# Kernel optimization log

Hardware: AMD Instinct MI355X
Metric: run time of the kernel (lower is better)

## Reference

```python
import jax, jax.numpy as jnp
import numpy as np

N, E, G = 25600, 409600, 128   # nodes, edges, graphs
IN, H, C = 200, 4, 64          # raw feat dim, heads, hidden_channels
IN2 = 2 * IN                   # after NaN-mask concat
BN_EPS = 1e-5

def _glorot(key, shape):
    lim = float(np.sqrt(6.0 / (shape[0] + shape[-1])))
    return jax.random.uniform(key, shape, jnp.float32, -lim, lim)

def setup_inputs():
    key = jax.random.key(0)
    k = iter(jax.random.split(key, 40))
    inp = {
        "x": jax.random.normal(next(k), (N, IN), jnp.float32),
        "edge_index": jax.random.randint(next(k), (2, E), 0, N, jnp.int32),
        "edge_attr": jax.random.normal(next(k), (E, 1), jnp.float32),
        "batch": jnp.repeat(jnp.arange(G, dtype=jnp.int32), N // G),
    }
    dims = [(IN2, H, C), (H * C, H, C), (H * C, 1, C)]
    for i, (din, h, c) in enumerate(dims):
        inp[f"W{i}"] = _glorot(next(k), (din, h * c))
        inp[f"as{i}"] = _glorot(next(k), (h, c))
        inp[f"ad{i}"] = _glorot(next(k), (h, c))
        inp[f"We{i}"] = _glorot(next(k), (1, h * c))
        inp[f"ae{i}"] = _glorot(next(k), (h, c))
        inp[f"b{i}"] = jnp.zeros((h * c,), jnp.float32)
    inp["bn_g"] = jnp.ones((H * C,), jnp.float32)
    inp["bn_b"] = jnp.zeros((H * C,), jnp.float32)
    inp["bn_m"] = jnp.zeros((H * C,), jnp.float32)
    inp["bn_v"] = jnp.ones((H * C,), jnp.float32)
    inp["cw1"] = _glorot(next(k), (C, C))
    inp["cb1"] = jnp.zeros((C,), jnp.float32)
    inp["cw2"] = _glorot(next(k), (C, 2))
    inp["cb2"] = jnp.zeros((2,), jnp.float32)
    return inp

def _gat(x, src, dst, ea, W, att_s, att_d, We, att_e, b, heads, ch):
    """PyG GATConv (edge_dim=1, add_self_loops=True, fill_value='mean', concat=True)."""
    n = x.shape[0]
    # self-loop edge_attr = mean of incoming edge_attr per destination node
    cnt = jax.ops.segment_sum(jnp.ones((ea.shape[0], 1), ea.dtype), dst, n)
    loop_ea = jax.ops.segment_sum(ea, dst, n) / jnp.maximum(cnt, 1.0)
    idx = jnp.arange(n, dtype=src.dtype)
    src = jnp.concatenate([src, idx])
    dst = jnp.concatenate([dst, idx])
    ea = jnp.concatenate([ea, loop_ea], axis=0)
    h = (x @ W).reshape(n, heads, ch)                      # [N,H,C]
    a_s = jnp.einsum('nhc,hc->nh', h, att_s)
    a_d = jnp.einsum('nhc,hc->nh', h, att_d)
    a_e = jnp.einsum('ehc,hc->eh', (ea @ We).reshape(-1, heads, ch), att_e)
    alpha = jax.nn.leaky_relu(a_s[src] + a_d[dst] + a_e, 0.2)   # [E',H]
    # segment softmax over destination neighborhoods
    m = jax.ops.segment_max(alpha, dst, n)
    ex = jnp.exp(alpha - m[dst])
    z = jax.ops.segment_sum(ex, dst, n)
    alpha = ex / (z[dst] + 1e-16)
    out = jax.ops.segment_sum(h[src] * alpha[:, :, None], dst, n)  # [N,H,C]
    return out.reshape(n, heads * ch) + b

def reference(x, edge_index, edge_attr, batch,
              W0, as0, ad0, We0, ae0, b0,
              W1, as1, ad1, We1, ae1, b1,
              W2, as2, ad2, We2, ae2, b2,
              bn_g, bn_b, bn_m, bn_v, cw1, cb1, cw2, cb2):
    nan_mask = jnp.isnan(x).astype(x.dtype)
    x = jnp.concatenate([jnp.nan_to_num(x), nan_mask], axis=-1)   # [N, 2*IN]
    edge_attr = jnp.nan_to_num(edge_attr)
    src, dst = edge_index[0], edge_index[1]
    for (W, a_s, a_d, We, a_e, b) in [(W0, as0, ad0, We0, ae0, b0),
                                      (W1, as1, ad1, We1, ae1, b1)]:
        x = _gat(x, src, dst, edge_attr, W, a_s, a_d, We, a_e, b, H, C)
        x = (x - bn_m) / jnp.sqrt(bn_v + BN_EPS) * bn_g + bn_b    # eval-mode BN
        x = jax.nn.relu(x)                                        # dropout = identity (eval)
    x = _gat(x, src, dst, edge_attr, W2, as2, ad2, We2, ae2, b2, 1, C)
    # global mean pool over graphs
    cnt = jax.ops.segment_sum(jnp.ones((x.shape[0], 1), x.dtype), batch, G)
    g = jax.ops.segment_sum(x, batch, G) / jnp.maximum(cnt, 1.0)  # [G, C]
    hdn = jax.nn.gelu(g @ cw1 + cb1, approximate=False)
    return hdn @ cw2 + cb2                                        # [G, 2]
```

## Files before the change

### kernel.cpp

```cpp
#include <hip/hip_runtime.h>
#include <hip/hip_bf16.h>

static const int kN  = 25600;
static const int kE  = 409600;
static const int kG  = 128;
static const int kNPG = 200;
static const int kIN = 200;
static const int kIN2 = 400;
static const int kHB = 64;
static const int kEPB = kE / kHB;
#define BN_EPS_ 1e-5f

typedef __attribute__((ext_vector_type(8))) short short8;
typedef __attribute__((ext_vector_type(4))) ushort us4;
typedef __attribute__((ext_vector_type(4))) float f32x4;

__device__ __forceinline__ float bu(ushort u) {
  union { float f; unsigned u32; } x; x.u32 = ((unsigned)u) << 16; return x.f;
}
__device__ __forceinline__ ushort f2u(float v) {
  __hip_bfloat16 t = __float2bfloat16(v);
  return *(ushort*)&t;
}
__device__ __forceinline__ float wredSum(float v) {
#pragma unroll
  for (int off = 1; off < 64; off <<= 1) v += __shfl_xor(v, off, 64);
  return v;
}
__device__ __forceinline__ float lrelu(float a) { return (a > 0.f) ? a : 0.2f * a; }

__global__ void k_pre(const float* __restrict__ x, ushort* __restrict__ x2,
                      const float* __restrict__ W0, ushort* __restrict__ Wt0,
                      const float* __restrict__ W1, ushort* __restrict__ Wt1,
                      const float* __restrict__ W2, ushort* __restrict__ Wt2,
                      const float* __restrict__ We0, const float* __restrict__ ae0,
                      const float* __restrict__ We1, const float* __restrict__ ae1,
                      const float* __restrict__ We2, const float* __restrict__ ae2,
                      float* __restrict__ wed) {
  int b = blockIdx.x, tid = threadIdx.x;
  if (b < 5000) {
    int i4 = (b * 256 + tid) * 4;
    int n = i4 / kIN, j = i4 - n * kIN;
    float4 v = *(const float4*)&x[i4];
    ushort o0[4], o1[4];
    float vv[4] = {v.x, v.y, v.z, v.w};
#pragma unroll
    for (int q = 0; q < 4; q++) {
      bool bad = (vv[q] != vv[q]);
      o0[q] = f2u(bad ? 0.f : vv[q]);
      o1[q] = f2u(bad ? 1.f : 0.f);
    }
    *(us4*)&x2[(size_t)n * kIN2 + j] = *(us4*)o0;
    *(us4*)&x2[(size_t)n * kIN2 + kIN + j] = *(us4*)o1;
    return;
  }
  int pb = b - 5000;
  if (pb >= 720) {
    int l = pb - 720;
    const float* We = (l == 0) ? We0 : (l == 1) ? We1 : We2;
    const float* ae = (l == 0) ? ae0 : (l == 1) ? ae1 : ae2;
    int n = (l == 2) ? 64 : 256;
    float v = (tid < n) ? We[tid] * ae[tid] : 0.f;
    v = wredSum(v);
    if ((tid & 63) == 0 && tid < n) wed[l * 4 + (tid >> 6)] = v;
    return;
  }
  int i = pb * 256 + tid;
  if (i < 102400) {
    int n = i / kIN2, k = i - n * kIN2;
    Wt0[(size_t)n * kIN2 + k] = f2u(W0[(size_t)k * 256 + n]);
  } else if (i < 102400 + 65536) {
    int j = i - 102400;
    int n = j >> 8, k = j & 255;
    Wt1[(size_t)n * 256 + k] = f2u(W1[(size_t)k * 256 + n]);
  } else {
    int j = i - 102400 - 65536;
    int n = j >> 8, k = j & 255;
    Wt2[(size_t)n * 256 + k] = f2u(W2[(size_t)k * 64 + n]);
  }
}

__global__ __launch_bounds__(1024) void k_hist(const int* __restrict__ ei,
                                               int* __restrict__ epos,
                                               int* __restrict__ blockcnt) {
  __shared__ int cnt[kN];
  int t = threadIdx.x, b = blockIdx.x;
  for (int i = t; i < kN; i += 1024) cnt[i] = 0;
  __syncthreads();
  int base = b * kEPB;
  for (int i = t; i < kEPB; i += 1024) {
    int e = base + i;
    int d = ei[kE + e];
    epos[e] = atomicAdd(&cnt[d], 1);
  }
  __syncthreads();
  for (int i = t; i < kN; i += 1024) blockcnt[(size_t)b * kN + i] = cnt[i];
}

__global__ void k_colscan(int* __restrict__ blockcnt, int* __restrict__ deg) {
  int n = blockIdx.x * 256 + threadIdx.x;
  int acc = 0;
#pragma unroll 8
  for (int b = 0; b < kHB; b++) {
    size_t idx = (size_t)b * kN + n;
    int v = blockcnt[idx];
    blockcnt[idx] = acc;
    acc += v;
  }
  deg[n] = acc;
}

__global__ void k_scan_all(const int* __restrict__ deg, int* __restrict__ rowp) {
  __shared__ int s[1024];
  int t = threadIdx.x;
  int base = t * 25;
  int loc[25];
  int sum = 0;
#pragma unroll
  for (int i = 0; i < 25; i++) { loc[i] = sum; sum += deg[base + i]; }
  s[t] = sum;
  __syncthreads();
  for (int off = 1; off < 1024; off <<= 1) {
    int v = (t >= off) ? s[t - off] : 0;
    __syncthreads();
    s[t] += v;
    __syncthreads();
  }
  int excl = s[t] - sum;
#pragma unroll
  for (int i = 0; i < 25; i++) rowp[base + i] = excl + loc[i];
}

__global__ void k_scatter_n(const int* __restrict__ ei, const float* __restrict__ ea,
                            const int* __restrict__ rowp, const int* __restrict__ epos,
                            const int* __restrict__ blockcnt,
                            int* __restrict__ esrc, float* __restrict__ eaC) {
  int e = blockIdx.x * blockDim.x + threadIdx.x;
  if (e >= kE) return;
  int d = ei[kE + e];
  int b = e / kEPB;
  int slot = rowp[d] + d + blockcnt[(size_t)b * kN + d] + epos[e];
  esrc[slot] = ei[e];
  float v = ea[e];
  if (v != v) v = 0.f;
  eaC[slot] = v;
}

#define GBK 64
#define GPAD 72

template <int BN, int MT>
__global__ __launch_bounds__(256) void k_gemm_f(const ushort* __restrict__ A,
                                                const ushort* __restrict__ Bt,
                                                ushort* __restrict__ C,
                                                const float* __restrict__ as_g,
                                                const float* __restrict__ ad_g,
                                                float* __restrict__ a_sg,
                                                float* __restrict__ a_dg, int K) {
  constexpr int MI = (BN == 256) ? (MT / 16) : 1;
  constexpr int H = (BN == 256) ? 4 : 1;
  __shared__ ushort As[MT * GPAD];
  __shared__ ushort Bs[BN * GPAD];
  int tid = threadIdx.x;
  int lane = tid & 63, w = tid >> 6;
  int l15 = lane & 15, l4 = lane >> 4;
  int row0 = blockIdx.y * MT;
  int wr = (BN == 256) ? 0 : (w * 16);
  int wc = (BN == 256) ? (w * 64) : 0;
  f32x4 acc[MI][4] = {};
  int ach = tid & 7, arow = tid >> 3;

  for (int kt = 0; kt < K; kt += GBK) {
    __syncthreads();
#pragma unroll
    for (int p = 0; p < MT / 32; p++) {
      int r = p * 32 + arow;
      int kg = kt + ach * 8;
      short8 v = {0, 0, 0, 0, 0, 0, 0, 0};
      if (kg < K) v = *(const short8*)&A[(size_t)(row0 + r) * K + kg];
      *(short8*)&As[r * GPAD + ach * 8] = v;
    }
#pragma unroll
    for (int p = 0; p < BN / 32; p++) {
      int r = p * 32 + arow;
      int kg = kt + ach * 8;
      short8 v = {0, 0, 0, 0, 0, 0, 0, 0};
      if (kg < K) v = *(const short8*)&Bt[(size_t)r * K + kg];
      *(short8*)&Bs[r * GPAD + ach * 8] = v;
    }
    __syncthreads();
#pragma unroll
    for (int kk = 0; kk < 2; kk++) {
      short8 af[MI], bf[4];
#pragma unroll
      for (int mi = 0; mi < MI; mi++)
        af[mi] = *(const short8*)&As[(wr + mi * 16 + l15) * GPAD + kk * 32 + l4 * 8];
#pragma unroll
      for (int ni = 0; ni < 4; ni++)
        bf[ni] = *(const short8*)&Bs[(wc + ni * 16 + l15) * GPAD + kk * 32 + l4 * 8];
#pragma unroll
      for (int mi = 0; mi < MI; mi++)
#pragma unroll
        for (int ni = 0; ni < 4; ni++)
          acc[mi][ni] = __builtin_amdgcn_mfma_f32_16x16x32_bf16(af[mi], bf[ni],
                                                                acc[mi][ni], 0, 0, 0);
    }
  }
#pragma unroll
  for (int mi = 0; mi < MI; mi++) {
    int rbase = row0 + wr + mi * 16 + l4 * 4;
#pragma unroll
    for (int ni = 0; ni < 4; ni++) {
      int col = wc + ni * 16 + l15;
#pragma unroll
      for (int r = 0; r < 4; r++)
        C[(size_t)(rbase + r) * BN + col] = f2u(acc[mi][ni][r]);
    }
  }
  float asv[4], adv[4];
#pragma unroll
  for (int ni = 0; ni < 4; ni++) {
    asv[ni] = as_g[wc + ni * 16 + l15];
    adv[ni] = ad_g[wc + ni * 16 + l15];
  }
  int hh = (BN == 256) ? w : 0;
#pragma unroll
  for (int mi = 0; mi < MI; mi++) {
#pragma unroll
    for (int r = 0; r < 4; r++) {
      float ps = 0.f, pd = 0.f;
#pragma unroll
      for (int ni = 0; ni < 4; ni++) {
        ps += acc[mi][ni][r] * asv[ni];
        pd += acc[mi][ni][r] * adv[ni];
      }
#pragma unroll
      for (int off = 1; off < 16; off <<= 1) {
        ps += __shfl_xor(ps, off, 64);
        pd += __shfl_xor(pd, off, 64);
      }
      if (l15 == 0) {
        int row = row0 + wr + mi * 16 + l4 * 4 + r;
        a_sg[row * H + hh] = ps;
        a_dg[row * H + hh] = pd;
      }
    }
  }
}

__global__ __launch_bounds__(256) void k_agg4(
    const ushort* __restrict__ hbuf, const int* __restrict__ rowp,
    const int* __restrict__ deg, const int* __restrict__ esrc,
    const float* __restrict__ eaC, const float* __restrict__ a_s,
    const float* __restrict__ a_d, const float* __restrict__ wed,
    const float* __restrict__ bias, const float* __restrict__ bng,
    const float* __restrict__ bnb, const float* __restrict__ bnm,
    const float* __restrict__ bnv, ushort* __restrict__ xout) {
  int tid = threadIdx.x;
  int w = tid >> 6, lane = tid & 63;
  int d = blockIdx.x * 4 + w;
  int start = rowp[d] + d;
  int dg = deg[d];
  int h = lane >> 4;
  float adh = a_d[d * 4 + h];
  float wdh = wed[h];

  int c0 = lane * 4;
  float a0 = 0.f, a1 = 0.f, a2 = 0.f, a3 = 0.f, sz = 0.f, sea = 0.f;
  int k = 0;
  for (; k + 4 <= dg; k += 4) {
    int s0 = esrc[start + k], s1 = esrc[start + k + 1];
    int s2 = esrc[start + k + 2], s3 = esrc[start + k + 3];
    float e0 = eaC[start + k], e1 = eaC[start + k + 1];
    float e2 = eaC[start + k + 2], e3 = eaC[start + k + 3];
    ushort4 v0 = *(const ushort4*)&hbuf[(size_t)s0 * 256 + c0];
    ushort4 v1 = *(const ushort4*)&hbuf[(size_t)s1 * 256 + c0];
    ushort4 v2 = *(const ushort4*)&hbuf[(size_t)s2 * 256 + c0];
    ushort4 v3 = *(const ushort4*)&hbuf[(size_t)s3 * 256 + c0];
    float w0 = __expf(lrelu(a_s[s0 * 4 + h] + adh + e0 * wdh));
    float w1 = __expf(lrelu(a_s[s1 * 4 + h] + adh + e1 * wdh));
    float w2 = __expf(lrelu(a_s[s2 * 4 + h] + adh + e2 * wdh));
    float w3 = __expf(lrelu(a_s[s3 * 4 + h] + adh + e3 * wdh));
    sea += (e0 + e1) + (e2 + e3);
    sz += (w0 + w1) + (w2 + w3);
    a0 += w0 * bu(v0.x) + w1 * bu(v1.x) + w2 * bu(v2.x) + w3 * bu(v3.x);
    a1 += w0 * bu(v0.y) + w1 * bu(v1.y) + w2 * bu(v2.y) + w3 * bu(v3.y);
    a2 += w0 * bu(v0.z) + w1 * bu(v1.z) + w2 * bu(v2.z) + w3 * bu(v3.z);
    a3 += w0 * bu(v0.w) + w1 * bu(v1.w) + w2 * bu(v2.w) + w3 * bu(v3.w);
  }
  for (; k < dg; k++) {
    int s0 = esrc[start + k];
    float e0 = eaC[start + k];
    ushort4 v0 = *(const ushort4*)&hbuf[(size_t)s0 * 256 + c0];
    float w0 = __expf(lrelu(a_s[s0 * 4 + h] + adh + e0 * wdh));
    sea += e0;
    sz += w0;
    a0 += w0 * bu(v0.x); a1 += w0 * bu(v0.y);
    a2 += w0 * bu(v0.z); a3 += w0 * bu(v0.w);
  }
  {
    float lea = sea / fmaxf((float)dg, 1.f);
    ushort4 v0 = *(const ushort4*)&hbuf[(size_t)d * 256 + c0];
    float w0 = __expf(lrelu(a_s[d * 4 + h] + adh + lea * wdh));
    sz += w0;
    a0 += w0 * bu(v0.x); a1 += w0 * bu(v0.y);
    a2 += w0 * bu(v0.z); a3 += w0 * bu(v0.w);
  }
  float winv = 1.f / (sz + 1e-16f);

  float4 bi = *(const float4*)&bias[c0];
  a0 = a0 * winv + bi.x; a1 = a1 * winv + bi.y;
  a2 = a2 * winv + bi.z; a3 = a3 * winv + bi.w;
  float4 g4 = *(const float4*)&bng[c0], b4 = *(const float4*)&bnb[c0];
  float4 m4 = *(const float4*)&bnm[c0], v4 = *(const float4*)&bnv[c0];
  a0 = fmaxf((a0 - m4.x) * rsqrtf(v4.x + BN_EPS_) * g4.x + b4.x, 0.f);
  a1 = fmaxf((a1 - m4.y) * rsqrtf(v4.y + BN_EPS_) * g4.y + b4.y, 0.f);
  a2 = fmaxf((a2 - m4.z) * rsqrtf(v4.z + BN_EPS_) * g4.z + b4.z, 0.f);
  a3 = fmaxf((a3 - m4.w) * rsqrtf(v4.w + BN_EPS_) * g4.w + b4.w, 0.f);
  ushort4 o = make_ushort4(f2u(a0), f2u(a1), f2u(a2), f2u(a3));
  *(ushort4*)&xout[(size_t)d * 256 + c0] = o;
}

__global__ __launch_bounds__(256) void k_agg1(
    const ushort* __restrict__ hbuf, const int* __restrict__ rowp,
    const int* __restrict__ deg, const int* __restrict__ esrc,
    const float* __restrict__ eaC, const float* __restrict__ a_s,
    const float* __restrict__ a_d, const float* __restrict__ wed,
    const float* __restrict__ bias, float* __restrict__ xout) {
  int tid = threadIdx.x;
  int w = tid >> 6, lane = tid & 63;
  int d = blockIdx.x * 4 + w;
  int start = rowp[d] + d;
  int dg = deg[d];
  float adh = a_d[d];
  float wdh = wed[0];

  float acc = 0.f, sz = 0.f, sea = 0.f;
  int k = 0;
  for (; k + 4 <= dg; k += 4) {
    int s0 = esrc[start + k], s1 = esrc[start + k + 1];
    int s2 = esrc[start + k + 2], s3 = esrc[start + k + 3];
    float e0 = eaC[start + k], e1 = eaC[start + k + 1];
    float e2 = eaC[start + k + 2], e3 = eaC[start + k + 3];
    float v0 = bu(hbuf[(size_t)s0 * 64 + lane]);
    float v1 = bu(hbuf[(size_t)s1 * 64 + lane]);
    float v2 = bu(hbuf[(size_t)s2 * 64 + lane]);
    float v3 = bu(hbuf[(size_t)s3 * 64 + lane]);
    float w0 = __expf(lrelu(a_s[s0] + adh + e0 * wdh));
    float w1 = __expf(lrelu(a_s[s1] + adh + e1 * wdh));
    float w2 = __expf(lrelu(a_s[s2] + adh + e2 * wdh));
    float w3 = __expf(lrelu(a_s[s3] + adh + e3 * wdh));
    sea += (e0 + e1) + (e2 + e3);
    sz += (w0 + w1) + (w2 + w3);
    acc += w0 * v0 + w1 * v1 + w2 * v2 + w3 * v3;
  }
  for (; k < dg; k++) {
    int s0 = esrc[start + k];
    float e0 = eaC[start + k];
    float w0 = __expf(lrelu(a_s[s0] + adh + e0 * wdh));
    sea += e0;
    sz += w0;
    acc += w0 * bu(hbuf[(size_t)s0 * 64 + lane]);
  }
  {
    float lea = sea / fmaxf((float)dg, 1.f);
    float w0 = __expf(lrelu(a_s[d] + adh + lea * wdh));
    sz += w0;
    acc += w0 * bu(hbuf[(size_t)d * 64 + lane]);
  }
  acc = acc / (sz + 1e-16f) + bias[lane];
  xout[(size_t)d * 64 + lane] = acc;
}

__global__ void k_poolhead(const float* __restrict__ xin,
                           const float* __restrict__ cw1, const float* __restrict__ cb1,
                           const float* __restrict__ cw2, const float* __restrict__ cb2,
                           float* __restrict__ out) {
  __shared__ float part[4][64];
  __shared__ float gb[64], hb[64];
  int g = blockIdx.x, tid = threadIdx.x;
  int c = tid & 63, w = tid >> 6;
  float acc = 0.f;
  size_t base = (size_t)g * kNPG * 64;
  for (int n = w; n < kNPG; n += 4) acc += xin[base + (size_t)n * 64 + c];
  part[w][c] = acc;
  __syncthreads();
  if (tid < 64) {
    float s = (part[0][c] + part[1][c]) + (part[2][c] + part[3][c]);
    gb[c] = s * (1.f / kNPG);
  }
  __syncthreads();
  if (tid < 64) {
    float s = cb1[c];
#pragma unroll 8
    for (int i = 0; i < 64; i++) s += gb[i] * cw1[i * 64 + c];
    s = 0.5f * s * (1.f + erff(s * 0.70710678118654752f));
    hb[c] = s;
  }
  __syncthreads();
  if (tid < 2) {
    float o = cb2[tid];
    for (int i = 0; i < 64; i++) o += hb[i] * cw2[i * 2 + tid];
    out[g * 2 + tid] = o;
  }
}


extern "C" void kernel_launch(void* const* d_in, const int* in_sizes, int n_in,
                              void* d_out, int out_size, void* d_ws, size_t ws_size,
                              hipStream_t stream) {
  (void)in_sizes; (void)n_in; (void)out_size; (void)ws_size;
  const float* x  = (const float*)d_in[0];
  const int* ei   = (const int*)d_in[1];
  const float* ea = (const float*)d_in[2];
  const float *W[3], *as_[3], *ad_[3], *We[3], *ae[3], *bi[3];
  for (int l = 0; l < 3; l++) {
    W[l]   = (const float*)d_in[4 + l * 6 + 0];
    as_[l] = (const float*)d_in[4 + l * 6 + 1];
    ad_[l] = (const float*)d_in[4 + l * 6 + 2];
    We[l]  = (const float*)d_in[4 + l * 6 + 3];
    ae[l]  = (const float*)d_in[4 + l * 6 + 4];
    bi[l]  = (const float*)d_in[4 + l * 6 + 5];
  }
  const float* bng = (const float*)d_in[22];
  const float* bnb = (const float*)d_in[23];
  const float* bnm = (const float*)d_in[24];
  const float* bnv = (const float*)d_in[25];
  const float* cw1 = (const float*)d_in[26];
  const float* cb1 = (const float*)d_in[27];
  const float* cw2 = (const float*)d_in[28];
  const float* cb2 = (const float*)d_in[29];

  char* p = (char*)d_ws;
  auto alloc = [&](size_t bytes) -> void* {
    void* r = (void*)p;
    p += (bytes + 255) & ~(size_t)255;
    return r;
  };
  ushort* x2b   = (ushort*)alloc((size_t)kN * kIN2 * 2);
  ushort* hbufb = (ushort*)alloc((size_t)kN * 256 * 2);
  ushort* xbA   = (ushort*)alloc((size_t)kN * 256 * 2);
  ushort* xbB   = (ushort*)alloc((size_t)kN * 256 * 2);
  float*  fbuf  = (float*)alloc((size_t)kN * 64 * 4);
  ushort* Wt0   = (ushort*)alloc((size_t)kIN2 * 256 * 2);
  ushort* Wt1   = (ushort*)alloc((size_t)256 * 256 * 2);
  ushort* Wt2   = (ushort*)alloc((size_t)256 * 64 * 2);
  float* a_s    = (float*)alloc((size_t)kN * 4 * 4);
  float* a_d    = (float*)alloc((size_t)kN * 4 * 4);
  int* rowp     = (int*)alloc((size_t)kN * 4);
  int* esrc     = (int*)alloc((size_t)(kE + kN) * 4);
  float* eaC    = (float*)alloc((size_t)(kE + kN) * 4);
  int* epos     = (int*)alloc((size_t)kE * 4);
  int* blockcnt = (int*)alloc((size_t)kHB * kN * 4);
  float* wed    = (float*)alloc(256);
  int* deg      = (int*)alloc((size_t)kN * 4);

  k_pre<<<5000 + 720 + 3, 256, 0, stream>>>(x, x2b, W[0], Wt0, W[1], Wt1,
                                            W[2], Wt2, We[0], ae[0], We[1], ae[1],
                                            We[2], ae[2], wed);
  k_hist<<<kHB, 1024, 0, stream>>>(ei, epos, blockcnt);
  k_colscan<<<kN / 256, 256, 0, stream>>>(blockcnt, deg);
  k_scan_all<<<1, 1024, 0, stream>>>(deg, rowp);
  k_scatter_n<<<(kE + 255) / 256, 256, 0, stream>>>(ei, ea, rowp, epos, blockcnt,
                                                    esrc, eaC);
  dim3 gg32(1, kN / 32);
  k_gemm_f<256, 32><<<gg32, 256, 0, stream>>>(x2b, Wt0, hbufb, as_[0], ad_[0],
                                              a_s, a_d, kIN2);
  k_agg4<<<kN / 4, 256, 0, stream>>>(hbufb, rowp, deg, esrc, eaC, a_s, a_d,
                                     &wed[0], bi[0], bng, bnb, bnm, bnv, xbA);
  k_gemm_f<256, 32><<<gg32, 256, 0, stream>>>(xbA, Wt1, hbufb, as_[1], ad_[1],
                                              a_s, a_d, 256);
  k_agg4<<<kN / 4, 256, 0, stream>>>(hbufb, rowp, deg, esrc, eaC, a_s, a_d,
                                     &wed[4], bi[1], bng, bnb, bnm, bnv, xbB);
  dim3 gg64(1, kN / 64);
  k_gemm_f<64, 64><<<gg64, 256, 0, stream>>>(xbB, Wt2, hbufb, as_[2], ad_[2],
                                             a_s, a_d, 256);
  k_agg1<<<kN / 4, 256, 0, stream>>>(hbufb, rowp, deg, esrc, eaC, a_s, a_d,
                                     &wed[8], bi[2], fbuf);
  k_poolhead<<<kG, 256, 0, stream>>>(fbuf, cw1, cb1, cw2, cb2, (float*)d_out);
}
```

Baseline: 329.1 us.

## Fold degree histogram into preprocessing kernel with global atomics; enlarge GEMM M tile

Replaces the per-block shared-memory histogram and column-scan kernels with global atomicAdd on deg, done by extra blocks appended to the preprocessing kernel after a memset. This removes two launches and the large blockcnt buffer, and simplifies slot computation in the scatter. It also switches the first two GEMMs from 32-row to 64-row tiles, halving the grid. Global atomics on contended degrees make CSR order nondeterministic, which can change float summation order, and the larger tile lowers block count and occupancy.

After: 326.8 us. About the same (-0.7%).

```diff
diff --git a/kernel.cpp b/kernel.cpp
--- a/kernel.cpp
+++ b/kernel.cpp
@@ -7,8 +7,6 @@
 static const int kNPG = 200;
 static const int kIN = 200;
 static const int kIN2 = 400;
-static const int kHB = 64;
-static const int kEPB = kE / kHB;
 #define BN_EPS_ 1e-5f
 
 typedef __attribute__((ext_vector_type(8))) short short8;
@@ -36,7 +34,9 @@
                       const float* __restrict__ We0, const float* __restrict__ ae0,
                       const float* __restrict__ We1, const float* __restrict__ ae1,
                       const float* __restrict__ We2, const float* __restrict__ ae2,
-                      float* __restrict__ wed) {
+                      float* __restrict__ wed,
+                      const int* __restrict__ ei, int* __restrict__ epos,
+                      int* __restrict__ deg) {
   int b = blockIdx.x, tid = threadIdx.x;
   if (b < 5000) {
     int i4 = (b * 256 + tid) * 4;
@@ -55,6 +55,12 @@
     return;
   }
   int pb = b - 5000;
+  if (pb >= 723) {
+    int e = (pb - 723) * 256 + tid;
+    int d = ei[kE + e];
+    epos[e] = atomicAdd(&deg[d], 1);
+    return;
+  }
   if (pb >= 720) {
     int l = pb - 720;
     const float* We = (l == 0) ? We0 : (l == 1) ? We1 : We2;
@@ -80,36 +86,6 @@
   }
 }
 
-__global__ __launch_bounds__(1024) void k_hist(const int* __restrict__ ei,
-                                               int* __restrict__ epos,
-                                               int* __restrict__ blockcnt) {
-  __shared__ int cnt[kN];
-  int t = threadIdx.x, b = blockIdx.x;
-  for (int i = t; i < kN; i += 1024) cnt[i] = 0;
-  __syncthreads();
-  int base = b * kEPB;
-  for (int i = t; i < kEPB; i += 1024) {
-    int e = base + i;
-    int d = ei[kE + e];
-    epos[e] = atomicAdd(&cnt[d], 1);
-  }
-  __syncthreads();
-  for (int i = t; i < kN; i += 1024) blockcnt[(size_t)b * kN + i] = cnt[i];
-}
-
-__global__ void k_colscan(int* __restrict__ blockcnt, int* __restrict__ deg) {
-  int n = blockIdx.x * 256 + threadIdx.x;
-  int acc = 0;
-#pragma unroll 8
-  for (int b = 0; b < kHB; b++) {
-    size_t idx = (size_t)b * kN + n;
-    int v = blockcnt[idx];
-    blockcnt[idx] = acc;
-    acc += v;
-  }
-  deg[n] = acc;
-}
-
 __global__ void k_scan_all(const int* __restrict__ deg, int* __restrict__ rowp) {
   __shared__ int s[1024];
   int t = threadIdx.x;
@@ -133,13 +109,11 @@
 
 __global__ void k_scatter_n(const int* __restrict__ ei, const float* __restrict__ ea,
                             const int* __restrict__ rowp, const int* __restrict__ epos,
-                            const int* __restrict__ blockcnt,
                             int* __restrict__ esrc, float* __restrict__ eaC) {
   int e = blockIdx.x * blockDim.x + threadIdx.x;
   if (e >= kE) return;
   int d = ei[kE + e];
-  int b = e / kEPB;
-  int slot = rowp[d] + d + blockcnt[(size_t)b * kN + d] + epos[e];
+  int slot = rowp[d] + d + epos[e];
   esrc[slot] = ei[e];
   float v = ea[e];
   if (v != v) v = 0.f;
@@ -451,25 +425,23 @@
   int* esrc     = (int*)alloc((size_t)(kE + kN) * 4);
   float* eaC    = (float*)alloc((size_t)(kE + kN) * 4);
   int* epos     = (int*)alloc((size_t)kE * 4);
-  int* blockcnt = (int*)alloc((size_t)kHB * kN * 4);
   float* wed    = (float*)alloc(256);
   int* deg      = (int*)alloc((size_t)kN * 4);
 
-  k_pre<<<5000 + 720 + 3, 256, 0, stream>>>(x, x2b, W[0], Wt0, W[1], Wt1,
-                                            W[2], Wt2, We[0], ae[0], We[1], ae[1],
-                                            We[2], ae[2], wed);
-  k_hist<<<kHB, 1024, 0, stream>>>(ei, epos, blockcnt);
-  k_colscan<<<kN / 256, 256, 0, stream>>>(blockcnt, deg);
+  hipMemsetAsync(deg, 0, (size_t)kN * 4, stream);
+  k_pre<<<5000 + 720 + 3 + 1600, 256, 0, stream>>>(
+      x, x2b, W[0], Wt0, W[1], Wt1, W[2], Wt2, We[0], ae[0], We[1], ae[1],
+      We[2], ae[2], wed, ei, epos, deg);
   k_scan_all<<<1, 1024, 0, stream>>>(deg, rowp);
-  k_scatter_n<<<(kE + 255) / 256, 256, 0, stream>>>(ei, ea, rowp, epos, blockcnt,
+  k_scatter_n<<<(kE + 255) / 256, 256, 0, stream>>>(ei, ea, rowp, epos,
                                                     esrc, eaC);
-  dim3 gg32(1, kN / 32);
-  k_gemm_f<256, 32><<<gg32, 256, 0, stream>>>(x2b, Wt0, hbufb, as_[0], ad_[0],
-                                              a_s, a_d, kIN2);
+  dim3 gg64m(1, kN / 64);
+  k_gemm_f<256, 64><<<gg64m, 256, 0, stream>>>(x2b, Wt0, hbufb, as_[0], ad_[0],
+                                               a_s, a_d, kIN2);
   k_agg4<<<kN / 4, 256, 0, stream>>>(hbufb, rowp, deg, esrc, eaC, a_s, a_d,
                                      &wed[0], bi[0], bng, bnb, bnm, bnv, xbA);
-  k_gemm_f<256, 32><<<gg32, 256, 0, stream>>>(xbA, Wt1, hbufb, as_[1], ad_[1],
-                                              a_s, a_d, 256);
+  k_gemm_f<256, 64><<<gg64m, 256, 0, stream>>>(xbA, Wt1, hbufb, as_[1], ad_[1],
+                                               a_s, a_d, 256);
   k_agg4<<<kN / 4, 256, 0, stream>>>(hbufb, rowp, deg, esrc, eaC, a_s, a_d,
                                      &wed[4], bi[1], bng, bnb, bnm, bnv, xbB);
   dim3 gg64(1, kN / 64);
```
